# Kernel tuning notes

Hardware: AMD Instinct MI355X
Metric: run time of the kernel (lower is better)

Reference implementation:

```python
import jax, jax.numpy as jnp
import numpy as np

EMBED_DIM = 1024

def setup_inputs() -> dict:
    key = jax.random.key(0)
    kx, kwq, kbq, kwk, kbk, kwv, kbv = jax.random.split(key, 7)
    d = EMBED_DIM
    s = 1.0 / np.sqrt(d)
    x = jax.random.normal(kx, (4, 2048, d), dtype=jnp.float32)
    # nn.Linear weights are [out, in]; we store transposed [in, out] for x @ W
    Wq = jax.random.uniform(kwq, (d, d), jnp.float32, -s, s)
    bq = jax.random.uniform(kbq, (d,), jnp.float32, -s, s)
    Wk = jax.random.uniform(kwk, (d, d), jnp.float32, -s, s)
    bk = jax.random.uniform(kbk, (d,), jnp.float32, -s, s)
    Wv = jax.random.uniform(kwv, (d, d), jnp.float32, -s, s)
    bv = jax.random.uniform(kbv, (d,), jnp.float32, -s, s)
    return {"x": x, "Wq": Wq, "bq": bq, "Wk": Wk, "bk": bk, "Wv": Wv, "bv": bv}

def reference(x, Wq, bq, Wk, bk, Wv, bv):
    d = x.shape[-1]
    q = x @ Wq + bq            # [B, S, D]
    k = x @ Wk + bk            # [B, S, D]
    v = x @ Wv + bv            # [B, S, D]
    scores = jnp.einsum('bsd,btd->bst', q, k) / jnp.sqrt(jnp.asarray(d, x.dtype))
    attn = jax.nn.softmax(scores, axis=-1)  # [B, S, S]
    return jnp.einsum('bst,btd->bsd', attn, v)
```

## Files before the change

### kernel.cpp

```cpp
#include <hip/hip_runtime.h>
#include <hip/hip_bf16.h>
#include <stdint.h>


typedef short bf16x8 __attribute__((ext_vector_type(8)));
typedef float f32x4 __attribute__((ext_vector_type(4)));
typedef unsigned short us4 __attribute__((ext_vector_type(4)));
typedef _Float16 h4 __attribute__((ext_vector_type(4)));
typedef unsigned short us;

#define B_ 4
#define S_ 2048
#define D_ 1024

__device__ __forceinline__ us f2bf(float f) {
  unsigned int u = __float_as_uint(f);
  unsigned int r = (u + 0x7fffu + ((u >> 16) & 1u)) >> 16;
  return (us)r;
}

__device__ __forceinline__ void gl2lds16(void* lds, const void* g) {
  __builtin_amdgcn_global_load_lds(
      (const __attribute__((address_space(1))) unsigned int*)(uintptr_t)g,
      (__attribute__((address_space(3))) unsigned int*)(uintptr_t)lds,
      16, 0, 0);
}

__device__ __forceinline__ void wait_vm6() {
  asm volatile("s_waitcnt vmcnt(6)" ::: "memory");
}
__device__ __forceinline__ void wait_vm0() {
  asm volatile("s_waitcnt vmcnt(0)" ::: "memory");
}
__device__ __forceinline__ void sbar() {
  __builtin_amdgcn_sched_barrier(0);
  __builtin_amdgcn_s_barrier();
  __builtin_amdgcn_sched_barrier(0);
}

template<int BM, int R0, int R1>
__device__ __forceinline__ void stageR(us* buf, const us* gA, size_t sA,
                                       const us* gB, size_t sB,
                                       int wave, int lane) {
  int slot = ((lane & 7) ^ (lane >> 3)) << 4;
  char* l = (char*)buf;
#pragma unroll
  for (int r = R0; r < R1; ++r) {
    int row = r * 64 + wave * 8 + (lane >> 3);
    const char* src;
    if (r * 64 < BM)
      src = (const char*)gA + (size_t)row * sA + slot;
    else
      src = (const char*)gB + (size_t)(row - BM) * sB + slot;
    gl2lds16(l + r * 8192 + wave * 1024, src);
  }
}

template<int EPI, int BM, int BN, int WMS, int WNS>
__global__ __launch_bounds__(512, 2) void gemm8p(
    const us* __restrict__ Aall, const us* __restrict__ Ball,
    size_t aBatch, size_t bBatch, int sAe, int sBe, int nt,
    const float* __restrict__ bq, const float* __restrict__ bk,
    const float* __restrict__ bv, void* __restrict__ outp) {
  __shared__ __align__(16) us lds[3][(BM + BN) * 64];
  int tid = threadIdx.x, lane = tid & 63, wave = tid >> 6;
  int wm = wave / WNS, wn = wave % WNS;
  int m0 = blockIdx.x * BM, n0 = blockIdx.y * BN;
  size_t bz = blockIdx.z;
  const us* gA = Aall + bz * aBatch + (size_t)m0 * sAe;
  const us* gB = Ball + bz * bBatch + (size_t)n0 * sBe;
  size_t sA = (size_t)sAe * 2, sB = (size_t)sBe * 2;

  stageR<BM, 0, 6>(lds[0], gA, sA, gB, sB, wave, lane);
  stageR<BM, 0, 6>(lds[1], gA + 64, sA, gB + 64, sB, wave, lane);

  int r15 = lane & 15, kg = lane >> 4, l7 = lane & 7;
  int x0 = (kg ^ l7) << 4;
  f32x4 acc[4][4] = {};

  for (int t = 0; t < nt; ++t) {
    if (t == nt - 1) wait_vm0(); else wait_vm6();
    sbar();
    const us* buf = lds[t % 3];
    us* nbuf = lds[(t + 2) % 3];
    bool dostage = (t + 2 < nt);
    const us* gA2 = gA + (size_t)(t + 2) * 64;
    const us* gB2 = gB + (size_t)(t + 2) * 64;
    const char* pa = (const char*)buf + (wm * 64 + r15) * 128;
    const char* pb = (const char*)buf + (BM + wn * 64 + r15) * 128;

    if (dostage) stageR<BM, 0, 3>(nbuf, gA2, sA, gB2, sB, wave, lane);
    bf16x8 A0[4], B0[4];
#pragma unroll
    for (int f = 0; f < 4; ++f) A0[f] = *(const bf16x8*)(pa + f * 2048 + x0);
#pragma unroll
    for (int f = 0; f < 4; ++f) B0[f] = *(const bf16x8*)(pb + f * 2048 + x0);
    __builtin_amdgcn_s_setprio(1);
#pragma unroll
    for (int fn = 0; fn < 4; ++fn)
#pragma unroll
      for (int fm = 0; fm < 4; ++fm)
        acc[fm][fn] = __builtin_amdgcn_mfma_f32_16x16x32_bf16(A0[fm], B0[fn], acc[fm][fn], 0, 0, 0);
    __builtin_amdgcn_s_setprio(0);

    if (dostage) stageR<BM, 3, 6>(nbuf, gA2, sA, gB2, sB, wave, lane);
    bf16x8 A1[4], B1[4];
#pragma unroll
    for (int f = 0; f < 4; ++f) A1[f] = *(const bf16x8*)(pa + f * 2048 + (x0 ^ 64));
#pragma unroll
    for (int f = 0; f < 4; ++f) B1[f] = *(const bf16x8*)(pb + f * 2048 + (x0 ^ 64));
    __builtin_amdgcn_s_setprio(1);
#pragma unroll
    for (int fn = 0; fn < 4; ++fn)
#pragma unroll
      for (int fm = 0; fm < 4; ++fm)
        acc[fm][fn] = __builtin_amdgcn_mfma_f32_16x16x32_bf16(A1[fm], B1[fn], acc[fm][fn], 0, 0, 0);
    __builtin_amdgcn_s_setprio(0);
  }

#pragma unroll
  for (int fm = 0; fm < 4; ++fm)
#pragma unroll
    for (int fn = 0; fn < 4; ++fn) {
      int col = n0 + wn * 64 + fn * 16 + r15;
      int row0 = m0 + wm * 64 + fm * 16 + ((lane >> 4) << 2);
      if constexpr (EPI == 0) {
        int mat = col >> 10;
        const float* bp = (mat == 0) ? bq : (mat == 1) ? bk : bv;
        float bb = bp[col & 1023];
        us* ob = (us*)outp + ((size_t)mat << 23);
#pragma unroll
        for (int r = 0; r < 4; ++r)
          ob[(size_t)(row0 + r) * D_ + (col & 1023)] = f2bf(acc[fm][fn][r] + bb);
      } else if constexpr (EPI == 1) {
        _Float16* sc = (_Float16*)outp + bz * (size_t)(S_ * S_);
#pragma unroll
        for (int r = 0; r < 4; ++r)
          sc[(size_t)(row0 + r) * S_ + col] = (_Float16)(acc[fm][fn][r] * 0.03125f);
      } else {
        float* ob = (float*)outp + bz * (size_t)(S_ * D_);
#pragma unroll
        for (int r = 0; r < 4; ++r)
          ob[(size_t)(row0 + r) * D_ + col] = acc[fm][fn][r];
      }
    }
}

__global__ __launch_bounds__(256) void wt_prep(const float* __restrict__ Wq,
                                               const float* __restrict__ Wk,
                                               const float* __restrict__ Wv,
                                               us* __restrict__ wtb) {
  __shared__ us hs[64][65];
  int mat = blockIdx.z;
  const float* W = (mat == 0) ? Wq : (mat == 1) ? Wk : Wv;
  int n0 = blockIdx.x * 64, k0 = blockIdx.y * 64;
  int tid = threadIdx.x;
#pragma unroll
  for (int i = 0; i < 16; ++i) {
    int idx = tid + i * 256;
    int r = idx >> 6, c = idx & 63;
    hs[r][c] = f2bf(W[(size_t)(k0 + r) * D_ + (n0 + c)]);
  }
  __syncthreads();
  us* o = wtb + ((size_t)mat << 20);
#pragma unroll
  for (int i = 0; i < 16; ++i) {
    int idx = tid + i * 256;
    int r = idx >> 6, c = idx & 63;
    o[(size_t)(n0 + r) * D_ + (k0 + c)] = hs[c][r];
  }
}

__global__ __launch_bounds__(256) void xcast(const float* __restrict__ x,
                                             us* __restrict__ xb) {
  size_t i = ((size_t)blockIdx.x * 256 + threadIdx.x) * 8;
  float4 f0 = *(const float4*)(x + i);
  float4 f1 = *(const float4*)(x + i + 4);
  float vals[8] = {f0.x, f0.y, f0.z, f0.w, f1.x, f1.y, f1.z, f1.w};
  union { bf16x8 v; us s_[8]; } H;
#pragma unroll
  for (int e = 0; e < 8; ++e) H.s_[e] = f2bf(vals[e]);
  *(bf16x8*)(xb + i) = H.v;
}

__global__ __launch_bounds__(256) void vtrans(const us* __restrict__ vin,
                                              us* __restrict__ vout) {
  int b = blockIdx.z;
  const us* vi = vin + (size_t)b * S_ * D_;
  us* vo = vout + (size_t)b * D_ * S_;
  int d0 = blockIdx.x * 64, t0 = blockIdx.y * 64;
  __shared__ us ts[64][72];
  int tid = threadIdx.x;
#pragma unroll
  for (int i = 0; i < 16; ++i) {
    int idx = tid + i * 256;
    int r = idx >> 6, c = idx & 63;
    ts[r][c] = vi[(size_t)(t0 + r) * D_ + d0 + c];
  }
  __syncthreads();
#pragma unroll
  for (int i = 0; i < 16; ++i) {
    int idx = tid + i * 256;
    int r = idx >> 6, c = idx & 63;
    vo[(size_t)(d0 + r) * S_ + t0 + c] = ts[c][r];
  }
}

__global__ __launch_bounds__(256) void softmax_k(const _Float16* __restrict__ scores,
                                                 us* __restrict__ pb) {
  int row = blockIdx.x, tid = threadIdx.x, lane = tid & 63, wave = tid >> 6;
  const _Float16* s = scores + (size_t)row * S_;
  h4 a4 = ((const h4*)s)[tid];
  h4 b4 = ((const h4*)s)[256 + tid];
  float a[8] = {(float)a4.x, (float)a4.y, (float)a4.z, (float)a4.w,
                (float)b4.x, (float)b4.y, (float)b4.z, (float)b4.w};
  float m = a[0];
#pragma unroll
  for (int e = 1; e < 8; ++e) m = fmaxf(m, a[e]);
#pragma unroll
  for (int o = 32; o; o >>= 1) m = fmaxf(m, __shfl_xor(m, o));
  __shared__ float red[4];
  if (lane == 0) red[wave] = m;
  __syncthreads();
  m = fmaxf(fmaxf(red[0], red[1]), fmaxf(red[2], red[3]));
  float p[8];
  float sum = 0.f;
#pragma unroll
  for (int e = 0; e < 8; ++e) { p[e] = expf(a[e] - m); sum += p[e]; }
#pragma unroll
  for (int o = 32; o; o >>= 1) sum += __shfl_xor(sum, o);
  __syncthreads();
  if (lane == 0) red[wave] = sum;
  __syncthreads();
  float inv = 1.0f / (red[0] + red[1] + red[2] + red[3]);
  us h[8];
#pragma unroll
  for (int e = 0; e < 8; ++e) h[e] = f2bf(p[e] * inv);
  size_t base = (size_t)row * S_;
  *(us4*)(pb + base + tid * 4) = (us4){h[0], h[1], h[2], h[3]};
  *(us4*)(pb + base + 1024 + tid * 4) = (us4){h[4], h[5], h[6], h[7]};
}

extern "C" void kernel_launch(void* const* d_in, const int* in_sizes, int n_in,
                              void* d_out, int out_size, void* d_ws, size_t ws_size,
                              hipStream_t stream) {
  const float* x  = (const float*)d_in[0];
  const float* Wq = (const float*)d_in[1];
  const float* bq = (const float*)d_in[2];
  const float* Wk = (const float*)d_in[3];
  const float* bk = (const float*)d_in[4];
  const float* Wv = (const float*)d_in[5];
  const float* bv = (const float*)d_in[6];
  float* out = (float*)d_out;
  char* ws = (char*)d_ws;
  const size_t MB = 1024 * 1024;
  us* qb   = (us*)(ws + 0 * MB);
  us* kb   = (us*)(ws + 16 * MB);
  us* vtmp = (us*)(ws + 32 * MB);
  us* wtb  = (us*)(ws + 48 * MB);
  us* xb   = (us*)(ws + 54 * MB);
  us* vtb  = (us*)(ws + 70 * MB);
  _Float16* scores = (_Float16*)(ws + 86 * MB);
  us* pb   = (us*)(ws + 118 * MB);
  (void)vtmp;

  wt_prep<<<dim3(16, 16, 3), 256, 0, stream>>>(Wq, Wk, Wv, wtb);
  xcast<<<dim3(4096), 256, 0, stream>>>(x, xb);
  gemm8p<0, 128, 256, 2, 4><<<dim3(64, 12, 1), 512, 0, stream>>>(
      xb, wtb, 0, 0, D_, D_, 16, bq, bk, bv, qb);
  vtrans<<<dim3(16, 32, 4), 256, 0, stream>>>(vtmp, vtb);
  gemm8p<1, 128, 256, 2, 4><<<dim3(16, 8, 4), 512, 0, stream>>>(
      qb, kb, (size_t)S_ * D_, (size_t)S_ * D_, D_, D_, 16,
      nullptr, nullptr, nullptr, scores);
  softmax_k<<<dim3(B_ * S_), 256, 0, stream>>>(scores, pb);
  gemm8p<2, 256, 128, 4, 2><<<dim3(8, 8, 4), 512, 0, stream>>>(
      pb, vtb, (size_t)S_ * S_, (size_t)D_ * S_, S_, S_, 32,
      nullptr, nullptr, nullptr, out);
}
```

Before: 158.1 us.

## Halve GEMM K-tile to 32 with new LDS swizzle and higher occupancy

The bf16 MFMA GEMM kernel now stages K-slices of 32 instead of 64 per pipeline step, which halves its LDS footprint. That lets launch bounds ask for 4 blocks per CU instead of 2. The LDS XOR swizzle is redesigned for 64-byte rows, and the vmcnt wait threshold and iteration counts are adjusted to match. The aim is more resident waves to hide memory latency, at the cost of twice as many barriers and loop iterations per output tile and possible register pressure from the tighter launch bound.

```diff
diff --git a/kernel.cpp b/kernel.cpp
--- a/kernel.cpp
+++ b/kernel.cpp
@@ -26,8 +26,8 @@
       16, 0, 0);
 }
 
-__device__ __forceinline__ void wait_vm6() {
-  asm volatile("s_waitcnt vmcnt(6)" ::: "memory");
+__device__ __forceinline__ void wait_vm3() {
+  asm volatile("s_waitcnt vmcnt(3)" ::: "memory");
 }
 __device__ __forceinline__ void wait_vm0() {
   asm volatile("s_waitcnt vmcnt(0)" ::: "memory");
@@ -38,31 +38,28 @@
   __builtin_amdgcn_sched_barrier(0);
 }
 
-template<int BM, int R0, int R1>
-__device__ __forceinline__ void stageR(us* buf, const us* gA, size_t sA,
-                                       const us* gB, size_t sB,
-                                       int wave, int lane) {
-  int slot = ((lane & 7) ^ (lane >> 3)) << 4;
+template<int BM>
+__device__ __forceinline__ void stage3(us* buf, const us* gA, size_t sA,
+                                       const us* gB, size_t sB, int wave, int lane) {
+  int slot = (((lane & 3) ^ ((lane >> 2) & 3) ^ ((lane >> 4) & 3)) << 4);
   char* l = (char*)buf;
 #pragma unroll
-  for (int r = R0; r < R1; ++r) {
-    int row = r * 64 + wave * 8 + (lane >> 3);
-    const char* src;
-    if (r * 64 < BM)
-      src = (const char*)gA + (size_t)row * sA + slot;
-    else
-      src = (const char*)gB + (size_t)(row - BM) * sB + slot;
+  for (int r = 0; r < 3; ++r) {
+    int row = r * 128 + wave * 16 + (lane >> 2);
+    const char* src = (r * 128 < BM)
+        ? (const char*)gA + (size_t)row * sA + slot
+        : (const char*)gB + (size_t)(row - BM) * sB + slot;
     gl2lds16(l + r * 8192 + wave * 1024, src);
   }
 }
 
-template<int EPI, int BM, int BN, int WMS, int WNS>
-__global__ __launch_bounds__(512, 2) void gemm8p(
+template<int EPI, int BM, int BN, int WNS>
+__global__ __launch_bounds__(512, 4) void gemm32(
     const us* __restrict__ Aall, const us* __restrict__ Ball,
     size_t aBatch, size_t bBatch, int sAe, int sBe, int nt,
     const float* __restrict__ bq, const float* __restrict__ bk,
     const float* __restrict__ bv, void* __restrict__ outp) {
-  __shared__ __align__(16) us lds[3][(BM + BN) * 64];
+  __shared__ __align__(16) us lds3[3][(BM + BN) * 32];
   int tid = threadIdx.x, lane = tid & 63, wave = tid >> 6;
   int wm = wave / WNS, wn = wave % WNS;
   int m0 = blockIdx.x * BM, n0 = blockIdx.y * BN;
@@ -71,50 +68,33 @@
   const us* gB = Ball + bz * bBatch + (size_t)n0 * sBe;
   size_t sA = (size_t)sAe * 2, sB = (size_t)sBe * 2;
 
-  stageR<BM, 0, 6>(lds[0], gA, sA, gB, sB, wave, lane);
-  stageR<BM, 0, 6>(lds[1], gA + 64, sA, gB + 64, sB, wave, lane);
-
-  int r15 = lane & 15, kg = lane >> 4, l7 = lane & 7;
-  int x0 = (kg ^ l7) << 4;
+  stage3<BM>(lds3[0], gA, sA, gB, sB, wave, lane);
+  stage3<BM>(lds3[1], gA + 32, sA, gB + 32, sB, wave, lane);
+
+  int r15 = lane & 15, kg = lane >> 4;
+  int x0 = ((kg ^ (r15 & 3) ^ ((r15 >> 2) & 3)) << 4);
   f32x4 acc[4][4] = {};
 
   for (int t = 0; t < nt; ++t) {
-    if (t == nt - 1) wait_vm0(); else wait_vm6();
+    if (t == nt - 1) wait_vm0(); else wait_vm3();
     sbar();
-    const us* buf = lds[t % 3];
-    us* nbuf = lds[(t + 2) % 3];
-    bool dostage = (t + 2 < nt);
-    const us* gA2 = gA + (size_t)(t + 2) * 64;
-    const us* gB2 = gB + (size_t)(t + 2) * 64;
-    const char* pa = (const char*)buf + (wm * 64 + r15) * 128;
-    const char* pb = (const char*)buf + (BM + wn * 64 + r15) * 128;
-
-    if (dostage) stageR<BM, 0, 3>(nbuf, gA2, sA, gB2, sB, wave, lane);
-    bf16x8 A0[4], B0[4];
-#pragma unroll
-    for (int f = 0; f < 4; ++f) A0[f] = *(const bf16x8*)(pa + f * 2048 + x0);
-#pragma unroll
-    for (int f = 0; f < 4; ++f) B0[f] = *(const bf16x8*)(pb + f * 2048 + x0);
+    const us* buf = lds3[t % 3];
+    if (t + 2 < nt)
+      stage3<BM>(lds3[(t + 2) % 3], gA + (size_t)(t + 2) * 32, sA,
+                 gB + (size_t)(t + 2) * 32, sB, wave, lane);
+    const char* pa = (const char*)buf + (size_t)(wm * 64 + r15) * 64;
+    const char* pb = (const char*)buf + (size_t)(BM + wn * 64 + r15) * 64;
+    bf16x8 Af[4], Bf[4];
+#pragma unroll
+    for (int f = 0; f < 4; ++f) Af[f] = *(const bf16x8*)(pa + f * 1024 + x0);
+#pragma unroll
+    for (int f = 0; f < 4; ++f) Bf[f] = *(const bf16x8*)(pb + f * 1024 + x0);
     __builtin_amdgcn_s_setprio(1);
 #pragma unroll
     for (int fn = 0; fn < 4; ++fn)
 #pragma unroll
       for (int fm = 0; fm < 4; ++fm)
-        acc[fm][fn] = __builtin_amdgcn_mfma_f32_16x16x32_bf16(A0[fm], B0[fn], acc[fm][fn], 0, 0, 0);
-    __builtin_amdgcn_s_setprio(0);
-
-    if (dostage) stageR<BM, 3, 6>(nbuf, gA2, sA, gB2, sB, wave, lane);
-    bf16x8 A1[4], B1[4];
-#pragma unroll
-    for (int f = 0; f < 4; ++f) A1[f] = *(const bf16x8*)(pa + f * 2048 + (x0 ^ 64));
-#pragma unroll
-    for (int f = 0; f < 4; ++f) B1[f] = *(const bf16x8*)(pb + f * 2048 + (x0 ^ 64));
-    __builtin_amdgcn_s_setprio(1);
-#pragma unroll
-    for (int fn = 0; fn < 4; ++fn)
-#pragma unroll
-      for (int fm = 0; fm < 4; ++fm)
-        acc[fm][fn] = __builtin_amdgcn_mfma_f32_16x16x32_bf16(A1[fm], B1[fn], acc[fm][fn], 0, 0, 0);
+        acc[fm][fn] = __builtin_amdgcn_mfma_f32_16x16x32_bf16(Af[fm], Bf[fn], acc[fm][fn], 0, 0, 0);
     __builtin_amdgcn_s_setprio(0);
   }
 
@@ -266,14 +246,14 @@
 
   wt_prep<<<dim3(16, 16, 3), 256, 0, stream>>>(Wq, Wk, Wv, wtb);
   xcast<<<dim3(4096), 256, 0, stream>>>(x, xb);
-  gemm8p<0, 128, 256, 2, 4><<<dim3(64, 12, 1), 512, 0, stream>>>(
-      xb, wtb, 0, 0, D_, D_, 16, bq, bk, bv, qb);
+  gemm32<0, 128, 256, 4><<<dim3(64, 12, 1), 512, 0, stream>>>(
+      xb, wtb, 0, 0, D_, D_, 32, bq, bk, bv, qb);
   vtrans<<<dim3(16, 32, 4), 256, 0, stream>>>(vtmp, vtb);
-  gemm8p<1, 128, 256, 2, 4><<<dim3(16, 8, 4), 512, 0, stream>>>(
-      qb, kb, (size_t)S_ * D_, (size_t)S_ * D_, D_, D_, 16,
+  gemm32<1, 128, 256, 4><<<dim3(16, 8, 4), 512, 0, stream>>>(
+      qb, kb, (size_t)S_ * D_, (size_t)S_ * D_, D_, D_, 32,
       nullptr, nullptr, nullptr, scores);
   softmax_k<<<dim3(B_ * S_), 256, 0, stream>>>(scores, pb);
-  gemm8p<2, 256, 128, 4, 2><<<dim3(8, 8, 4), 512, 0, stream>>>(
-      pb, vtb, (size_t)S_ * S_, (size_t)D_ * S_, S_, S_, 32,
+  gemm32<2, 256, 128, 2><<<dim3(8, 8, 4), 512, 0, stream>>>(
+      pb, vtb, (size_t)S_ * S_, (size_t)D_ * S_, S_, S_, 64,
       nullptr, nullptr, nullptr, out);
 }
```

Result: slower. 172.7 us (+9.2%).

## Add 256x256 GEMM kernel for QKV and QK^T, fuse V transpose into epilogue

Applied to the files above, without the earlier changes.

Adds a new 256x256-tile GEMM with a five-slot half-K LDS ring and finer-grained staging interleaved with MFMA phases. It is used for the QKV projection and the score GEMM. The QKV epilogue now writes V directly in transposed layout, which removes the separate vtrans kernel and its extra pass over memory. The larger tiles raise data reuse per block but use more LDS and registers, give fewer blocks to fill the device, and turn the V stores into strided writes.

```diff
diff --git a/kernel.cpp b/kernel.cpp
--- a/kernel.cpp
+++ b/kernel.cpp
@@ -26,16 +26,125 @@
       16, 0, 0);
 }
 
-__device__ __forceinline__ void wait_vm6() {
-  asm volatile("s_waitcnt vmcnt(6)" ::: "memory");
-}
-__device__ __forceinline__ void wait_vm0() {
-  asm volatile("s_waitcnt vmcnt(0)" ::: "memory");
-}
-__device__ __forceinline__ void sbar() {
-  __builtin_amdgcn_sched_barrier(0);
-  __builtin_amdgcn_s_barrier();
-  __builtin_amdgcn_sched_barrier(0);
+__device__ __forceinline__ void sched_fence() { __builtin_amdgcn_sched_barrier(0); }
+__device__ __forceinline__ void barrier_f() {
+  sched_fence(); __builtin_amdgcn_s_barrier(); sched_fence();
+}
+
+template<int EPI>
+__global__ __launch_bounds__(512, 2) void gemm256(
+    const us* __restrict__ Aall, const us* __restrict__ Ball,
+    size_t aBatch, size_t bBatch, int sAe, int sBe, int nt,
+    const float* __restrict__ bq, const float* __restrict__ bk,
+    const float* __restrict__ bv, void* __restrict__ outp,
+    us* __restrict__ vtb) {
+  __shared__ __align__(16) us lds[5 * 16384];
+  const int tid = threadIdx.x, lane = tid & 63, wave = tid >> 6;
+  const int wm = wave >> 2, wn = wave & 3;
+  const int m0 = blockIdx.x * 256, n0 = blockIdx.y * 256;
+  const size_t bz = blockIdx.z;
+  const char* gA = (const char*)(Aall + bz * aBatch + (size_t)m0 * sAe);
+  const char* gB = (const char*)(Ball + bz * bBatch + (size_t)n0 * sBe);
+  const size_t sA = (size_t)sAe * 2, sB = (size_t)sBe * 2;
+
+  const int r15 = lane & 15, kg = lane >> 4;
+  const int srcslot = ((lane & 7) ^ (lane >> 3)) << 4;
+  const int ldl = lane >> 3;
+  const int brow = (wn & 1) * 64;
+  const int nh = 2 * nt;
+
+  auto stage = [&](int h, int c) {
+    char* dst = (char*)lds + (h % 5) * 32768 +
+                (c < 2 ? c * 8192 : 16384 + (c - 2) * 8192) + wave * 1024;
+    int row = (h & 1) * 128 + (c < 2 ? c * 64 : (c - 2) * 64) + wave * 8 + ldl;
+    const char* src = (c < 2 ? gA + (size_t)row * sA : gB + (size_t)row * sB) +
+                      (size_t)(h >> 1) * 128 + srcslot;
+    gl2lds16(dst, src);
+  };
+
+#pragma unroll
+  for (int h = 0; h < 3; ++h)
+#pragma unroll
+    for (int c = 0; c < 4; ++c) stage(h, c);
+  asm volatile("s_waitcnt vmcnt(4)" ::: "memory");
+  barrier_f();
+
+  f32x4 acc[8][4] = {};
+  for (int t = 0; t < nt; ++t) {
+    const char* hbA = (const char*)lds + ((2 * t + wm) % 5) * 32768;
+    const char* hbB = (const char*)lds + ((2 * t + (wn >> 1)) % 5) * 32768 + 16384;
+    const int hs_base = 2 * t + 3;
+    bf16x8 Br[4];
+#pragma unroll
+    for (int p = 0; p < 4; ++p) {
+      const int kh = p >> 1, mq = p & 1;
+      bf16x8 Ar[4];
+#pragma unroll
+      for (int f = 0; f < 4; ++f) {
+        int lr = (mq * 4 + f) * 16 + r15;
+        Ar[f] = *(const bf16x8*)(hbA + lr * 128 +
+                                 ((((kh << 2) | kg) ^ (lr & 7)) << 4));
+      }
+      if (mq == 0) {
+#pragma unroll
+        for (int n = 0; n < 4; ++n) {
+          int lr = brow + n * 16 + r15;
+          Br[n] = *(const bf16x8*)(hbB + lr * 128 +
+                                   ((((kh << 2) | kg) ^ (lr & 7)) << 4));
+        }
+      }
+      {
+        int cp = p * 2;
+        int h1 = hs_base + (cp >> 2);
+        if (h1 < nh) stage(h1, cp & 3);
+        int h2 = hs_base + ((cp + 1) >> 2);
+        if (h2 < nh) stage(h2, (cp + 1) & 3);
+      }
+      barrier_f();
+      __builtin_amdgcn_s_setprio(1);
+#pragma unroll
+      for (int n = 0; n < 4; ++n)
+#pragma unroll
+        for (int f = 0; f < 4; ++f)
+          acc[mq * 4 + f][n] = __builtin_amdgcn_mfma_f32_16x16x32_bf16(
+              Ar[f], Br[n], acc[mq * 4 + f][n], 0, 0, 0);
+      __builtin_amdgcn_s_setprio(0);
+      if (p == 3) {
+        if (t <= nt - 3) asm volatile("s_waitcnt vmcnt(4)" ::: "memory");
+        else             asm volatile("s_waitcnt vmcnt(0)" ::: "memory");
+      }
+      barrier_f();
+    }
+  }
+
+#pragma unroll
+  for (int fm = 0; fm < 8; ++fm)
+#pragma unroll
+    for (int fn = 0; fn < 4; ++fn) {
+      int col = n0 + wn * 64 + fn * 16 + r15;
+      int row0 = m0 + wm * 128 + fm * 16 + ((lane >> 4) << 2);
+      if constexpr (EPI == 0) {
+        int mat = col >> 10;
+        const float* bp = (mat == 0) ? bq : (mat == 1) ? bk : bv;
+        float bb = bp[col & 1023];
+        if (mat < 2) {
+          us* ob = (us*)outp + ((size_t)mat << 23);
+#pragma unroll
+          for (int r = 0; r < 4; ++r)
+            ob[(size_t)(row0 + r) * D_ + (col & 1023)] = f2bf(acc[fm][fn][r] + bb);
+        } else {
+          int b = row0 >> 11, trow = row0 & 2047, dcol = col & 1023;
+          us4 v4 = {f2bf(acc[fm][fn][0] + bb), f2bf(acc[fm][fn][1] + bb),
+                    f2bf(acc[fm][fn][2] + bb), f2bf(acc[fm][fn][3] + bb)};
+          *(us4*)(vtb + (size_t)b * D_ * S_ + (size_t)dcol * S_ + trow) = v4;
+        }
+      } else {
+        _Float16* sc = (_Float16*)outp + bz * (size_t)(S_ * S_);
+#pragma unroll
+        for (int r = 0; r < 4; ++r)
+          sc[(size_t)(row0 + r) * S_ + col] = (_Float16)(acc[fm][fn][r] * 0.03125f);
+      }
+    }
 }
 
 template<int BM, int R0, int R1>
@@ -60,8 +169,7 @@
 __global__ __launch_bounds__(512, 2) void gemm8p(
     const us* __restrict__ Aall, const us* __restrict__ Ball,
     size_t aBatch, size_t bBatch, int sAe, int sBe, int nt,
-    const float* __restrict__ bq, const float* __restrict__ bk,
-    const float* __restrict__ bv, void* __restrict__ outp) {
+    void* __restrict__ outp) {
   __shared__ __align__(16) us lds[3][(BM + BN) * 64];
   int tid = threadIdx.x, lane = tid & 63, wave = tid >> 6;
   int wm = wave / WNS, wn = wave % WNS;
@@ -79,15 +187,16 @@
   f32x4 acc[4][4] = {};
 
   for (int t = 0; t < nt; ++t) {
-    if (t == nt - 1) wait_vm0(); else wait_vm6();
-    sbar();
+    if (t == nt - 1) asm volatile("s_waitcnt vmcnt(0)" ::: "memory");
+    else             asm volatile("s_waitcnt vmcnt(6)" ::: "memory");
+    barrier_f();
     const us* buf = lds[t % 3];
-    us* nbuf = lds[(t + 2) % 3];
+    us* nbuf = (us*)lds[(t + 2) % 3];
     bool dostage = (t + 2 < nt);
     const us* gA2 = gA + (size_t)(t + 2) * 64;
     const us* gB2 = gB + (size_t)(t + 2) * 64;
-    const char* pa = (const char*)buf + (wm * 64 + r15) * 128;
-    const char* pb = (const char*)buf + (BM + wn * 64 + r15) * 128;
+    const char* pa = (const char*)buf + (size_t)(wm * 64 + r15) * 128;
+    const char* pb = (const char*)buf + (size_t)(BM + wn * 64 + r15) * 128;
 
     if (dostage) stageR<BM, 0, 3>(nbuf, gA2, sA, gB2, sB, wave, lane);
     bf16x8 A0[4], B0[4];
@@ -124,25 +233,10 @@
     for (int fn = 0; fn < 4; ++fn) {
       int col = n0 + wn * 64 + fn * 16 + r15;
       int row0 = m0 + wm * 64 + fm * 16 + ((lane >> 4) << 2);
-      if constexpr (EPI == 0) {
-        int mat = col >> 10;
-        const float* bp = (mat == 0) ? bq : (mat == 1) ? bk : bv;
-        float bb = bp[col & 1023];
-        us* ob = (us*)outp + ((size_t)mat << 23);
-#pragma unroll
-        for (int r = 0; r < 4; ++r)
-          ob[(size_t)(row0 + r) * D_ + (col & 1023)] = f2bf(acc[fm][fn][r] + bb);
-      } else if constexpr (EPI == 1) {
-        _Float16* sc = (_Float16*)outp + bz * (size_t)(S_ * S_);
-#pragma unroll
-        for (int r = 0; r < 4; ++r)
-          sc[(size_t)(row0 + r) * S_ + col] = (_Float16)(acc[fm][fn][r] * 0.03125f);
-      } else {
-        float* ob = (float*)outp + bz * (size_t)(S_ * D_);
-#pragma unroll
-        for (int r = 0; r < 4; ++r)
-          ob[(size_t)(row0 + r) * D_ + col] = acc[fm][fn][r];
-      }
+      float* ob = (float*)outp + bz * (size_t)(S_ * D_);
+#pragma unroll
+      for (int r = 0; r < 4; ++r)
+        ob[(size_t)(row0 + r) * D_ + col] = acc[fm][fn][r];
     }
 }
 
@@ -181,29 +275,6 @@
 #pragma unroll
   for (int e = 0; e < 8; ++e) H.s_[e] = f2bf(vals[e]);
   *(bf16x8*)(xb + i) = H.v;
-}
-
-__global__ __launch_bounds__(256) void vtrans(const us* __restrict__ vin,
-                                              us* __restrict__ vout) {
-  int b = blockIdx.z;
-  const us* vi = vin + (size_t)b * S_ * D_;
-  us* vo = vout + (size_t)b * D_ * S_;
-  int d0 = blockIdx.x * 64, t0 = blockIdx.y * 64;
-  __shared__ us ts[64][72];
-  int tid = threadIdx.x;
-#pragma unroll
-  for (int i = 0; i < 16; ++i) {
-    int idx = tid + i * 256;
-    int r = idx >> 6, c = idx & 63;
-    ts[r][c] = vi[(size_t)(t0 + r) * D_ + d0 + c];
-  }
-  __syncthreads();
-#pragma unroll
-  for (int i = 0; i < 16; ++i) {
-    int idx = tid + i * 256;
-    int r = idx >> 6, c = idx & 63;
-    vo[(size_t)(d0 + r) * S_ + t0 + c] = ts[c][r];
-  }
 }
 
 __global__ __launch_bounds__(256) void softmax_k(const _Float16* __restrict__ scores,
@@ -255,25 +326,21 @@
   char* ws = (char*)d_ws;
   const size_t MB = 1024 * 1024;
   us* qb   = (us*)(ws + 0 * MB);
-  us* kb   = (us*)(ws + 16 * MB);
-  us* vtmp = (us*)(ws + 32 * MB);
+  us* vtb  = (us*)(ws + 32 * MB);
   us* wtb  = (us*)(ws + 48 * MB);
   us* xb   = (us*)(ws + 54 * MB);
-  us* vtb  = (us*)(ws + 70 * MB);
-  _Float16* scores = (_Float16*)(ws + 86 * MB);
-  us* pb   = (us*)(ws + 118 * MB);
-  (void)vtmp;
+  _Float16* scores = (_Float16*)(ws + 70 * MB);
+  us* pb   = (us*)(ws + 102 * MB);
+  us* kb   = (us*)(ws + 16 * MB);
 
   wt_prep<<<dim3(16, 16, 3), 256, 0, stream>>>(Wq, Wk, Wv, wtb);
   xcast<<<dim3(4096), 256, 0, stream>>>(x, xb);
-  gemm8p<0, 128, 256, 2, 4><<<dim3(64, 12, 1), 512, 0, stream>>>(
-      xb, wtb, 0, 0, D_, D_, 16, bq, bk, bv, qb);
-  vtrans<<<dim3(16, 32, 4), 256, 0, stream>>>(vtmp, vtb);
-  gemm8p<1, 128, 256, 2, 4><<<dim3(16, 8, 4), 512, 0, stream>>>(
+  gemm256<0><<<dim3(32, 12, 1), 512, 0, stream>>>(
+      xb, wtb, 0, 0, D_, D_, 16, bq, bk, bv, qb, vtb);
+  gemm256<1><<<dim3(8, 8, 4), 512, 0, stream>>>(
       qb, kb, (size_t)S_ * D_, (size_t)S_ * D_, D_, D_, 16,
-      nullptr, nullptr, nullptr, scores);
+      nullptr, nullptr, nullptr, scores, nullptr);
   softmax_k<<<dim3(B_ * S_), 256, 0, stream>>>(scores, pb);
   gemm8p<2, 256, 128, 4, 2><<<dim3(8, 8, 4), 512, 0, stream>>>(
-      pb, vtb, (size_t)S_ * S_, (size_t)D_ * S_, S_, S_, 32,
-      nullptr, nullptr, nullptr, out);
-}
+      pb, vtb, (size_t)S_ * S_, (size_t)D_ * S_, S_, S_, 32, out);
+}
```

New measurement: 169.9 us. 1.07x slower.
